# Kernel tuning notes

Measured on AMD Instinct MI355X. Metric: run time of the kernel, lower is better.

Reference implementation:

```python
import jax, jax.numpy as jnp
import numpy as np

N, F, C, E = 1024, 64, 4, 32768
H = 256       # MLP hidden width
C_OUT = 4     # new edge channels produced by nn_edge


def setup_inputs() -> dict:
    key = jax.random.key(0)
    ks = jax.random.split(key, 12)
    x = jax.random.normal(ks[0], (N, F), dtype=jnp.float32)
    edge_index = jax.random.randint(ks[1], (C, 2, E), 0, N)
    edge_weight = jax.random.uniform(ks[2], (C, E), dtype=jnp.float32)
    s_n1 = 1.0 / np.sqrt(C * F)
    s_n2 = 1.0 / np.sqrt(H)
    s_e1 = 1.0 / np.sqrt(C + 2 * F)
    return {
        "x": x,
        "edge_index": edge_index,
        "edge_weight": edge_weight,
        "Wn1": jax.random.normal(ks[3], (C * F, H), dtype=jnp.float32) * s_n1,
        "bn1": jnp.zeros((H,), jnp.float32),
        "Wn2": jax.random.normal(ks[4], (H, F), dtype=jnp.float32) * s_n2,
        "bn2": jnp.zeros((F,), jnp.float32),
        "We1": jax.random.normal(ks[5], (C + 2 * F, H), dtype=jnp.float32) * s_e1,
        "be1": jnp.zeros((H,), jnp.float32),
        "We2": jax.random.normal(ks[6], (H, C_OUT), dtype=jnp.float32) * s_n2,
        "be2": jnp.zeros((C_OUT,), jnp.float32),
        "eps": jnp.zeros((), jnp.float32),
    }


def reference(x, edge_index, edge_weight, Wn1, bn1, Wn2, bn2, We1, be1, We2, be2, eps):
    # ---- MCGNN: per-channel edge-weighted scatter-add aggregation ----
    def agg_one(ei, w):
        # ei: [2,E] (row0 = source j, row1 = target i); w: [E]
        msg = x[ei[0]] * w[:, None]                       # [E,F]
        return jax.ops.segment_sum(msg, ei[1], num_segments=N)  # [N,F]

    agg = jax.vmap(agg_one)(edge_index, edge_weight)      # [C,N,F]
    out_cat = agg + (1.0 + eps) * x                       # broadcast self term
    h = out_cat.transpose(1, 0, 2).reshape(N, C * F)      # [N, C*F]
    x_next = jax.nn.relu(h @ Wn1 + bn1) @ Wn2 + bn2       # [N,F]

    # ---- EDPGNN: dense adjacency per channel + broadcast x_i/x_j ----
    def dense_adj(ei, w):
        return jnp.zeros((N, N), x.dtype).at[ei[0], ei[1]].add(w)

    a = jax.vmap(dense_adj)(edge_index, edge_weight)      # [C,N,N]
    a = a.transpose(1, 2, 0)                              # [N,N,C]
    x_i = jnp.broadcast_to(x_next[:, None, :], (N, N, F))
    x_j = jnp.broadcast_to(x_next[None, :, :], (N, N, F))
    feat = jnp.concatenate([a, x_i, x_j], axis=2).reshape(N * N, C + 2 * F)
    adj_out = (jax.nn.relu(feat @ We1 + be1) @ We2 + be2).reshape(N, N, C_OUT)
    return adj_out
```

## Files before the change

kernel.cpp:

```cpp
#include <hip/hip_runtime.h>

#define NN 1024
#define FF 64
#define CC 4
#define EE 32768
#define HH 256

#define OFF_ADENSE 0u
#define OFF_CNT    4194304u
#define OFF_MASK   4198400u
#define OFF_OFFS   4231168u
#define OFF_CURSOR 4235268u
#define OFF_SRTS   4239364u
#define OFF_SRTW   4370436u
#define OFF_P      4501508u
#define OFF_Q      4763652u
#define OFF_QT     5025796u

__global__ __launch_bounds__(256)
void k_count(const int* __restrict__ ei, int* __restrict__ cnt,
             float4* __restrict__ adense4)
{
    unsigned t = blockIdx.x * 256u + threadIdx.x;
    unsigned e = t & (EE - 1u);
    unsigned c = t >> 15;
    int dst = ei[c * 2 * EE + EE + e];
    atomicAdd(&cnt[c * NN + dst], 1);

    const unsigned base = blockIdx.x * 2048u + threadIdx.x;
    const float4 z = make_float4(0.f, 0.f, 0.f, 0.f);
#pragma unroll
    for (int u = 0; u < 8; ++u)
        adense4[base + u * 256u] = z;
}

__global__ __launch_bounds__(256)
void k_scan(const int* __restrict__ cnt, int* __restrict__ offs, int* __restrict__ cursor)
{
    __shared__ int wsum[4];
    const int t = threadIdx.x;
    int c[16];
    int s = 0;
    const int4* cp = (const int4*)(cnt + t * 16);
#pragma unroll
    for (int u = 0; u < 4; ++u) {
        int4 v = cp[u];
        c[u * 4 + 0] = v.x; c[u * 4 + 1] = v.y; c[u * 4 + 2] = v.z; c[u * 4 + 3] = v.w;
        s += v.x + v.y + v.z + v.w;
    }
    int incl = s;
#pragma unroll
    for (int d = 1; d < 64; d <<= 1) {
        int v = __shfl_up(incl, d, 64);
        if ((t & 63) >= d) incl += v;
    }
    const int w = t >> 6;
    if ((t & 63) == 63) wsum[w] = incl;
    __syncthreads();
    int base = incl - s;
    for (int ww = 0; ww < w; ++ww) base += wsum[ww];
    int run = base;
#pragma unroll
    for (int u = 0; u < 16; ++u) {
        offs[t * 16 + u] = run;
        cursor[t * 16 + u] = run;
        run += c[u];
    }
    if (t == 255) offs[4096] = run;
}

__global__ __launch_bounds__(256)
void k_bucket_adj(const int* __restrict__ ei, const float* __restrict__ ew,
                  int* __restrict__ cursor, int* __restrict__ srt_src,
                  float* __restrict__ srt_w, float* __restrict__ adense,
                  unsigned* __restrict__ mask)
{
    unsigned t = blockIdx.x * 256u + threadIdx.x;
    unsigned e = t & (EE - 1u);
    unsigned c = t >> 15;
    int src = ei[c * 2 * EE + e];
    int dst = ei[c * 2 * EE + EE + e];
    float w = ew[c * EE + e];
    int pos = atomicAdd(&cursor[c * NN + dst], 1);
    srt_src[pos] = src;
    srt_w[pos] = w;
    unsigned pair = (unsigned)src * NN + (unsigned)dst;
    atomicAdd(&adense[(size_t)pair * CC + c], w);
    atomicOr(&mask[pair >> 5], 1u << (pair & 31u));
}

__global__ __launch_bounds__(1024)
void k_node(const float* __restrict__ x, const int* __restrict__ offs,
            const int* __restrict__ srt_src, const float* __restrict__ srt_w,
            const float* __restrict__ Wn1, const float* __restrict__ bn1,
            const float* __restrict__ Wn2, const float* __restrict__ bn2,
            const float* __restrict__ We1, const float* __restrict__ be1,
            const float* __restrict__ epsp,
            float* __restrict__ P, float* __restrict__ Q,
            float* __restrict__ QT)
{
    __shared__ float hval[4][256];
    __shared__ float hidl[4][256];
    __shared__ float part[4][4][64];
    __shared__ float xnl[4][64];
    const int tid = threadIdx.x;
    const int n0 = blockIdx.x * 4;

    {
        const int w = tid >> 6, lane = tid & 63;
        const int c = w & 3, nn = w >> 2;
        const int g = c * NN + (n0 + nn);
        const int beg = offs[g], end = offs[g + 1];
        float acc = 0.f;
        for (int k = beg; k < end; ++k)
            acc += x[srt_src[k] * FF + lane] * srt_w[k];
        const float ope = 1.0f + epsp[0];
        hval[nn][c * 64 + lane] = acc + ope * x[(n0 + nn) * FF + lane];
    }
    __syncthreads();

    {
        const int nn = tid >> 8, h = tid & 255;
        float acc = bn1[h];
#pragma unroll 8
        for (int k = 0; k < 256; ++k)
            acc += hval[nn][k] * Wn1[k * 256 + h];
        hidl[nn][h] = fmaxf(acc, 0.f);
    }
    __syncthreads();

    {
        const int kq = tid >> 8, nn = (tid >> 6) & 3, f = tid & 63;
        float p = 0.f;
#pragma unroll 8
        for (int k = kq * 64; k < kq * 64 + 64; ++k)
            p += hidl[nn][k] * Wn2[k * 64 + f];
        part[kq][nn][f] = p;
    }
    __syncthreads();
    if (tid < 256) {
        const int nn = tid >> 6, f = tid & 63;
        xnl[nn][f] = bn2[f] + part[0][nn][f] + part[1][nn][f]
                             + part[2][nn][f] + part[3][nn][f];
    }
    __syncthreads();

    {
        const int r = tid >> 8, h = tid & 255;
        float p = be1[h], q = 0.f;
#pragma unroll 8
        for (int f = 0; f < 64; ++f) {
            float xv = xnl[r][f];
            p += xv * We1[(4 + f) * 256 + h];
            q += xv * We1[(68 + f) * 256 + h];
        }
        P[(n0 + r) * 256 + h] = p;
        Q[(n0 + r) * 256 + h] = q;
        QT[((unsigned)(h >> 2) * NN + (unsigned)(n0 + r)) * 4u + (h & 3)] = q;
    }
}

__global__ __launch_bounds__(256, 4)
void k_edge_mlp(const float* __restrict__ P, const float* __restrict__ Q,
                const float4* __restrict__ QTP, const float* __restrict__ adense,
                const unsigned* __restrict__ mask, const float* __restrict__ We1,
                const float* __restrict__ We2, const float* __restrict__ be2,
                float* __restrict__ out)
{
    __shared__ float4 delta[512];
    __shared__ int nzlist[512];
    __shared__ int lcnt;

    const int tid = threadIdx.x;
    const int w = tid >> 6, lane = tid & 63;
    const int iBase = blockIdx.y * 8, jBase = blockIdx.x * 64;
    const int j = jBase + lane;
    const int i0 = __builtin_amdgcn_readfirstlane(iBase + w * 2);

    if (tid == 0) lcnt = 0;
    __syncthreads();

    unsigned nzbits = 0;
#pragma unroll
    for (int ii = 0; ii < 2; ++ii) {
        const unsigned mw = mask[(unsigned)(i0 + ii) * 32u + ((unsigned)j >> 5)];
        if ((mw >> (j & 31)) & 1u) {
            nzbits |= 1u << ii;
            int idx = atomicAdd(&lcnt, 1);
            nzlist[idx] = (w * 2 + ii) * 64 + lane;
        }
    }
    __syncthreads();

    const float4* P4  = (const float4*)P;
    const float4* W24 = (const float4*)We2;

    float4 acc0 = make_float4(0.f, 0.f, 0.f, 0.f);
    float4 acc1 = make_float4(0.f, 0.f, 0.f, 0.f);
    for (int hq = 0; hq < 64; ++hq) {
        const float4 qv  = QTP[hq * NN + j];
        const float4 pv0 = P4[(size_t)i0 * 64 + hq];
        const float4 pv1 = P4[(size_t)(i0 + 1) * 64 + hq];
        const float4 w20 = W24[hq * 4 + 0];
        const float4 w21 = W24[hq * 4 + 1];
        const float4 w22 = W24[hq * 4 + 2];
        const float4 w23 = W24[hq * 4 + 3];
        {
            const float v0 = fmaxf(pv0.x + qv.x, 0.f);
            const float v1 = fmaxf(pv0.y + qv.y, 0.f);
            const float v2 = fmaxf(pv0.z + qv.z, 0.f);
            const float v3 = fmaxf(pv0.w + qv.w, 0.f);
            acc0.x += v0 * w20.x + v1 * w21.x + v2 * w22.x + v3 * w23.x;
            acc0.y += v0 * w20.y + v1 * w21.y + v2 * w22.y + v3 * w23.y;
            acc0.z += v0 * w20.z + v1 * w21.z + v2 * w22.z + v3 * w23.z;
            acc0.w += v0 * w20.w + v1 * w21.w + v2 * w22.w + v3 * w23.w;
        }
        {
            const float v0 = fmaxf(pv1.x + qv.x, 0.f);
            const float v1 = fmaxf(pv1.y + qv.y, 0.f);
            const float v2 = fmaxf(pv1.z + qv.z, 0.f);
            const float v3 = fmaxf(pv1.w + qv.w, 0.f);
            acc1.x += v0 * w20.x + v1 * w21.x + v2 * w22.x + v3 * w23.x;
            acc1.y += v0 * w20.y + v1 * w21.y + v2 * w22.y + v3 * w23.y;
            acc1.z += v0 * w20.z + v1 * w21.z + v2 * w22.z + v3 * w23.z;
            acc1.w += v0 * w20.w + v1 * w21.w + v2 * w22.w + v3 * w23.w;
        }
    }

    {
        const int nfix = lcnt;
        for (int pi = w; pi < nfix; pi += 4) {
            const int lij = nzlist[pi];
            const int gi = iBase + (lij >> 6), gj = jBase + (lij & 63);
            const float4 a = *(const float4*)(adense + ((size_t)gi * NN + gj) * 4);
            float o0 = 0.f, o1 = 0.f, o2 = 0.f, o3 = 0.f;
#pragma unroll
            for (int u = 0; u < 4; ++u) {
                const int h = u * 64 + lane;
                float s = a.x * We1[0 * 256 + h] + a.y * We1[1 * 256 + h]
                        + a.z * We1[2 * 256 + h] + a.w * We1[3 * 256 + h];
                float v = fmaxf(P[gi * 256 + h] + Q[gj * 256 + h] + s, 0.f);
                const float4 w2 = W24[h];
                o0 += v * w2.x; o1 += v * w2.y; o2 += v * w2.z; o3 += v * w2.w;
            }
#pragma unroll
            for (int d = 32; d > 0; d >>= 1) {
                o0 += __shfl_down(o0, d, 64);
                o1 += __shfl_down(o1, d, 64);
                o2 += __shfl_down(o2, d, 64);
                o3 += __shfl_down(o3, d, 64);
            }
            if (lane == 0)
                delta[lij] = make_float4(o0, o1, o2, o3);
        }
    }
    __syncthreads();

    const float4 b2 = *(const float4*)be2;
#pragma unroll
    for (int ii = 0; ii < 2; ++ii) {
        const int lij = (w * 2 + ii) * 64 + lane;
        const float4 dfx = delta[lij];
        const float4 av = ii ? acc1 : acc0;
        const bool nzf = (nzbits >> ii) & 1u;
        float4 o;
        o.x = (nzf ? dfx.x : av.x) + b2.x;
        o.y = (nzf ? dfx.y : av.y) + b2.y;
        o.z = (nzf ? dfx.z : av.z) + b2.z;
        o.w = (nzf ? dfx.w : av.w) + b2.w;
        *(float4*)(out + ((size_t)(i0 + ii) * NN + j) * 4) = o;
    }
}

extern "C" void kernel_launch(void* const* d_in, const int* in_sizes, int n_in,
                              void* d_out, int out_size, void* d_ws, size_t ws_size,
                              hipStream_t stream)
{
    (void)in_sizes; (void)n_in; (void)out_size; (void)ws_size;
    const float* x   = (const float*)d_in[0];
    const int*   ei  = (const int*)d_in[1];
    const float* ew  = (const float*)d_in[2];
    const float* Wn1 = (const float*)d_in[3];
    const float* bn1 = (const float*)d_in[4];
    const float* Wn2 = (const float*)d_in[5];
    const float* bn2 = (const float*)d_in[6];
    const float* We1 = (const float*)d_in[7];
    const float* be1 = (const float*)d_in[8];
    const float* We2 = (const float*)d_in[9];
    const float* be2 = (const float*)d_in[10];
    const float* eps = (const float*)d_in[11];
    float* out = (float*)d_out;

    float*    ws     = (float*)d_ws;
    float*    adense = ws + OFF_ADENSE;
    int*      cnt    = (int*)(ws + OFF_CNT);
    unsigned* mask   = (unsigned*)(ws + OFF_MASK);
    int*      offs   = (int*)(ws + OFF_OFFS);
    int*      cursor = (int*)(ws + OFF_CURSOR);
    int*      srts   = (int*)(ws + OFF_SRTS);
    float*    srtw   = ws + OFF_SRTW;
    float*    Pb     = ws + OFF_P;
    float*    Qb     = ws + OFF_Q;
    float*    QTb    = ws + OFF_QT;

    (void)hipMemsetAsync((void*)cnt, 0, (size_t)(4096 + 32768) * sizeof(int), stream);

    k_count     <<<(CC * EE) / 256, 256, 0, stream>>>(ei, cnt, (float4*)adense);
    k_scan      <<<1, 256, 0, stream>>>(cnt, offs, cursor);
    k_bucket_adj<<<(CC * EE) / 256, 256, 0, stream>>>(ei, ew, cursor, srts, srtw,
                                                      adense, mask);
    k_node      <<<NN / 4, 1024, 0, stream>>>(x, offs, srts, srtw,
                                              Wn1, bn1, Wn2, bn2, We1, be1, eps,
                                              Pb, Qb, QTb);

    dim3 g(NN / 64, NN / 8);
    k_edge_mlp<<<g, 256, 0, stream>>>(Pb, Qb, (const float4*)QTb, adense, mask,
                                      We1, We2, be2, out);
}
```

Measured before the change: 220.5 us.

## Skip dense adjacency clear by zeroing touched entries after use; one node per block

The full clear of the 16 MB dense adjacency buffer is now skipped whenever the previous call's scan total is found in the workspace. Instead, the edge MLP kernel zeroes each nonzero adjacency entry after reading it. This removes a large memory write per call, but it depends on the workspace persisting between calls and on that sentinel check, so uninitialized or corrupted workspace could give wrong results. The node kernel also changes from 4 nodes per 1024-thread block to 1 node per 256-thread block, giving more, smaller blocks.

```diff
diff --git a/kernel.cpp b/kernel.cpp
--- a/kernel.cpp
+++ b/kernel.cpp
@@ -19,7 +19,7 @@
 
 __global__ __launch_bounds__(256)
 void k_count(const int* __restrict__ ei, int* __restrict__ cnt,
-             float4* __restrict__ adense4)
+             float4* __restrict__ adense4, const int* __restrict__ offs)
 {
     unsigned t = blockIdx.x * 256u + threadIdx.x;
     unsigned e = t & (EE - 1u);
@@ -27,11 +27,13 @@
     int dst = ei[c * 2 * EE + EE + e];
     atomicAdd(&cnt[c * NN + dst], 1);
 
-    const unsigned base = blockIdx.x * 2048u + threadIdx.x;
-    const float4 z = make_float4(0.f, 0.f, 0.f, 0.f);
-#pragma unroll
-    for (int u = 0; u < 8; ++u)
-        adense4[base + u * 256u] = z;
+    if (offs[4096] != CC * EE) {
+        const unsigned base = blockIdx.x * 2048u + threadIdx.x;
+        const float4 z = make_float4(0.f, 0.f, 0.f, 0.f);
+#pragma unroll
+        for (int u = 0; u < 8; ++u)
+            adense4[base + u * 256u] = z;
+    }
 }
 
 __global__ __launch_bounds__(256)
@@ -89,7 +91,7 @@
     atomicOr(&mask[pair >> 5], 1u << (pair & 31u));
 }
 
-__global__ __launch_bounds__(1024)
+__global__ __launch_bounds__(256)
 void k_node(const float* __restrict__ x, const int* __restrict__ offs,
             const int* __restrict__ srt_src, const float* __restrict__ srt_w,
             const float* __restrict__ Wn1, const float* __restrict__ bn1,
@@ -99,70 +101,67 @@
             float* __restrict__ P, float* __restrict__ Q,
             float* __restrict__ QT)
 {
-    __shared__ float hval[4][256];
-    __shared__ float hidl[4][256];
-    __shared__ float part[4][4][64];
-    __shared__ float xnl[4][64];
+    __shared__ float hval[256];
+    __shared__ float hidl[256];
+    __shared__ float part[4][64];
+    __shared__ float xnl[64];
     const int tid = threadIdx.x;
-    const int n0 = blockIdx.x * 4;
-
-    {
-        const int w = tid >> 6, lane = tid & 63;
-        const int c = w & 3, nn = w >> 2;
-        const int g = c * NN + (n0 + nn);
+    const int n = blockIdx.x;
+
+    {
+        const int c = tid >> 6, lane = tid & 63;
+        const int g = c * NN + n;
         const int beg = offs[g], end = offs[g + 1];
         float acc = 0.f;
         for (int k = beg; k < end; ++k)
             acc += x[srt_src[k] * FF + lane] * srt_w[k];
         const float ope = 1.0f + epsp[0];
-        hval[nn][c * 64 + lane] = acc + ope * x[(n0 + nn) * FF + lane];
-    }
-    __syncthreads();
-
-    {
-        const int nn = tid >> 8, h = tid & 255;
+        hval[c * 64 + lane] = acc + ope * x[n * FF + lane];
+    }
+    __syncthreads();
+
+    {
+        const int h = tid;
         float acc = bn1[h];
 #pragma unroll 8
         for (int k = 0; k < 256; ++k)
-            acc += hval[nn][k] * Wn1[k * 256 + h];
-        hidl[nn][h] = fmaxf(acc, 0.f);
-    }
-    __syncthreads();
-
-    {
-        const int kq = tid >> 8, nn = (tid >> 6) & 3, f = tid & 63;
+            acc += hval[k] * Wn1[k * 256 + h];
+        hidl[h] = fmaxf(acc, 0.f);
+    }
+    __syncthreads();
+
+    {
+        const int kq = tid >> 6, f = tid & 63;
         float p = 0.f;
 #pragma unroll 8
         for (int k = kq * 64; k < kq * 64 + 64; ++k)
-            p += hidl[nn][k] * Wn2[k * 64 + f];
-        part[kq][nn][f] = p;
-    }
-    __syncthreads();
-    if (tid < 256) {
-        const int nn = tid >> 6, f = tid & 63;
-        xnl[nn][f] = bn2[f] + part[0][nn][f] + part[1][nn][f]
-                             + part[2][nn][f] + part[3][nn][f];
-    }
-    __syncthreads();
-
-    {
-        const int r = tid >> 8, h = tid & 255;
+            p += hidl[k] * Wn2[k * 64 + f];
+        part[kq][f] = p;
+    }
+    __syncthreads();
+    if (tid < 64)
+        xnl[tid] = bn2[tid] + part[0][tid] + part[1][tid]
+                            + part[2][tid] + part[3][tid];
+    __syncthreads();
+
+    {
+        const int h = tid;
         float p = be1[h], q = 0.f;
 #pragma unroll 8
         for (int f = 0; f < 64; ++f) {
-            float xv = xnl[r][f];
+            float xv = xnl[f];
             p += xv * We1[(4 + f) * 256 + h];
             q += xv * We1[(68 + f) * 256 + h];
         }
-        P[(n0 + r) * 256 + h] = p;
-        Q[(n0 + r) * 256 + h] = q;
-        QT[((unsigned)(h >> 2) * NN + (unsigned)(n0 + r)) * 4u + (h & 3)] = q;
+        P[n * 256 + h] = p;
+        Q[n * 256 + h] = q;
+        QT[((unsigned)(h >> 2) * NN + (unsigned)n) * 4u + (h & 3)] = q;
     }
 }
 
 __global__ __launch_bounds__(256, 4)
 void k_edge_mlp(const float* __restrict__ P, const float* __restrict__ Q,
-                const float4* __restrict__ QTP, const float* __restrict__ adense,
+                const float4* __restrict__ QTP, float* __restrict__ adense,
                 const unsigned* __restrict__ mask, const float* __restrict__ We1,
                 const float* __restrict__ We2, const float* __restrict__ be2,
                 float* __restrict__ out)
@@ -232,7 +231,8 @@
         for (int pi = w; pi < nfix; pi += 4) {
             const int lij = nzlist[pi];
             const int gi = iBase + (lij >> 6), gj = jBase + (lij & 63);
-            const float4 a = *(const float4*)(adense + ((size_t)gi * NN + gj) * 4);
+            float* ap = adense + ((size_t)gi * NN + gj) * 4;
+            const float4 a = *(const float4*)ap;
             float o0 = 0.f, o1 = 0.f, o2 = 0.f, o3 = 0.f;
 #pragma unroll
             for (int u = 0; u < 4; ++u) {
@@ -250,8 +250,10 @@
                 o2 += __shfl_down(o2, d, 64);
                 o3 += __shfl_down(o3, d, 64);
             }
-            if (lane == 0)
+            if (lane == 0) {
                 delta[lij] = make_float4(o0, o1, o2, o3);
+                *(float4*)ap = make_float4(0.f, 0.f, 0.f, 0.f);
+            }
         }
     }
     __syncthreads();
@@ -305,13 +307,13 @@
 
     (void)hipMemsetAsync((void*)cnt, 0, (size_t)(4096 + 32768) * sizeof(int), stream);
 
-    k_count     <<<(CC * EE) / 256, 256, 0, stream>>>(ei, cnt, (float4*)adense);
+    k_count     <<<(CC * EE) / 256, 256, 0, stream>>>(ei, cnt, (float4*)adense, offs);
     k_scan      <<<1, 256, 0, stream>>>(cnt, offs, cursor);
     k_bucket_adj<<<(CC * EE) / 256, 256, 0, stream>>>(ei, ew, cursor, srts, srtw,
                                                       adense, mask);
-    k_node      <<<NN / 4, 1024, 0, stream>>>(x, offs, srts, srtw,
-                                              Wn1, bn1, Wn2, bn2, We1, be1, eps,
-                                              Pb, Qb, QTb);
+    k_node      <<<NN, 256, 0, stream>>>(x, offs, srts, srtw,
+                                         Wn1, bn1, Wn2, bn2, We1, be1, eps,
+                                         Pb, Qb, QTb);
 
     dim3 g(NN / 64, NN / 8);
     k_edge_mlp<<<g, 256, 0, stream>>>(Pb, Qb, (const float4*)QTb, adense, mask,
```

Result: no change. 224.6 us (+1.8%).
